# Kernel tuning notes

Measured on AMD Instinct MI355X. Metric: run time of the kernel, lower is better.

## Reference

```python
import jax, jax.numpy as jnp
import numpy as np

ORDER = 64
DT = 1.0 / 2048.0
L, BATCH, SIZE = 2048, 8, 64


def _hippo_legt(N):
    # HiPPO-LegT (LMU) continuous-time transition, as in s4 repo transition()
    Q = np.arange(N, dtype=np.float64)
    R = (2 * Q + 1) ** 0.5
    j, i = np.meshgrid(Q, Q)
    A = R[:, None] * np.where(i < j, (-1.0) ** (i - j), 1.0) * R[None, :]
    B = R[:, None]
    return -A, B


def _bilinear_discretize(A, B, dt):
    # scipy.signal.cont2discrete(..., method='bilinear')
    N = A.shape[0]
    I = np.eye(N)
    M = np.linalg.inv(I - (dt / 2.0) * A)
    Ad = M @ (I + (dt / 2.0) * A)
    Bd = M @ (dt * B)
    return Ad, Bd


def setup_inputs() -> dict:
    key = jax.random.key(0)
    inputs = jax.random.normal(key, (L, BATCH, SIZE), dtype=jnp.float32)
    Ac, Bc = _hippo_legt(ORDER)
    Ad, Bd = _bilinear_discretize(Ac, Bc, DT)
    return {
        "inputs": inputs,
        "A": jnp.asarray(Ad, dtype=jnp.float32),   # (order, order) discrete transition
        "Bm": jnp.asarray(Bd, dtype=jnp.float32),  # (order, 1) discrete input matrix
    }


def reference(inputs, A, Bm):
    # inputs: (L, B, S); A: (N, N); Bm: (N, 1)
    # u = F.linear(inputs.unsqueeze(-1), Bm): u[l,b,s,n] = inputs[l,b,s] * Bm[n,0]
    u = inputs[..., None] * Bm[:, 0]  # (L, B, S, N)

    # parallel_unroll_recursive computes x_t = A x_{t-1} + u_t with x_{-1} = 0
    def step(x, u_t):
        x_new = jnp.einsum('nm,bsm->bsn', A, x) + u_t
        return x_new, x_new

    x0 = jnp.zeros((inputs.shape[1], inputs.shape[2], A.shape[0]), dtype=inputs.dtype)
    _, out = jax.lax.scan(step, x0, u)
    return out  # (L, B, S, N)
```

## Files before the change

### kernel.cpp

```cpp
#include <hip/hip_runtime.h>


typedef _Float16 f16;
typedef __attribute__((ext_vector_type(8))) _Float16 f16x8;
typedef __attribute__((ext_vector_type(4))) float f32x4;

__global__ __launch_bounds__(1024) void kA_pow(
    const float* __restrict__ A, const float* __restrict__ Bm,
    const float* __restrict__ inp,
    float* __restrict__ A64, float* __restrict__ Kv,
    f16* __restrict__ W16, f16* __restrict__ R16)
{
  __shared__ __align__(16) char sA[92160];
  int t = threadIdx.x;

  if (blockIdx.x >= 64) {
    float (*tile)[132] = (float (*)[132])sA;
    int bb = blockIdx.x - 64;
    int j = bb >> 2, qb = (bb & 3) * 128;
    {
      int k = t >> 4, seg = (t & 15) * 8;
      const float* src = inp + j * 32768 + k * 512 + qb + seg;
      *(f32x4*)(&tile[k][seg])     = *(const f32x4*)(src);
      *(f32x4*)(&tile[k][seg + 4]) = *(const f32x4*)(src + 4);
    }
    __syncthreads();
    {
      int q = t & 127, ks8 = (t >> 7) * 8;
      f16 tmp[8];
      #pragma unroll
      for (int kk = 0; kk < 8; ++kk)
        tmp[kk] = (f16)tile[ks8 + kk][q];
      *(f16x8*)(R16 + ((size_t)(j * 512 + qb + q)) * 256 + ks8) =
          *(const f16x8*)tmp;
    }
    return;
  }

  f16 (*Ah)[72]  = (f16 (*)[72])(sA + 0 * 9216);
  f16 (*Al)[72]  = (f16 (*)[72])(sA + 1 * 9216);
  f16 (*B0h)[72] = (f16 (*)[72])(sA + 2 * 9216);
  f16 (*B0l)[72] = (f16 (*)[72])(sA + 3 * 9216);
  f16 (*B1h)[72] = (f16 (*)[72])(sA + 4 * 9216);
  f16 (*B1l)[72] = (f16 (*)[72])(sA + 5 * 9216);
  f16 (*Y8h)[72] = (f16 (*)[72])(sA + 6 * 9216);
  f16 (*Y8l)[72] = (f16 (*)[72])(sA + 7 * 9216);
  f16 (*Ybh)[72] = (f16 (*)[72])(sA + 8 * 9216);
  f16 (*Ybl)[72] = (f16 (*)[72])(sA + 9 * 9216);

  int tau = blockIdx.x;
  int e = tau + 1;
  int a = e >> 3, b = e & 7;
  int wave = t >> 6, lane = t & 63;
  int tn = wave >> 2, tm = wave & 3;
  int kg = lane >> 4, fr = lane & 15;

  auto mm = [&](f16 (*Ph)[72], f16 (*Pl)[72], f16 (*Qh)[72], f16 (*Ql)[72],
                f16 (*Dh)[72], f16 (*Dl)[72]) {
    f32x4 acc = {};
    #pragma unroll
    for (int kk = 0; kk < 2; ++kk) {
      f16x8 ah = *(const f16x8*)&Ph[tn * 16 + fr][kk * 32 + kg * 8];
      f16x8 al = *(const f16x8*)&Pl[tn * 16 + fr][kk * 32 + kg * 8];
      f16x8 bh = *(const f16x8*)&Qh[tm * 16 + fr][kk * 32 + kg * 8];
      f16x8 bl = *(const f16x8*)&Ql[tm * 16 + fr][kk * 32 + kg * 8];
      acc = __builtin_amdgcn_mfma_f32_16x16x32_f16(ah, bh, acc, 0, 0, 0);
      acc = __builtin_amdgcn_mfma_f32_16x16x32_f16(ah, bl, acc, 0, 0, 0);
      acc = __builtin_amdgcn_mfma_f32_16x16x32_f16(al, bh, acc, 0, 0, 0);
    }
    #pragma unroll
    for (int r = 0; r < 4; ++r) {
      float v = acc[r];
      f16 h = (f16)v, l = (f16)(v - (float)h);
      Dh[tn * 16 + kg * 4 + r][tm * 16 + fr] = h;
      Dl[tn * 16 + kg * 4 + r][tm * 16 + fr] = l;
    }
    __syncthreads();
  };
  auto cpy2 = [&](f16 (*Sh)[72], f16 (*Sl)[72], f16 (*Dh)[72], f16 (*Dl)[72]) {
    const unsigned* sh = (const unsigned*)Sh; unsigned* dh = (unsigned*)Dh;
    const unsigned* sl = (const unsigned*)Sl; unsigned* dl = (unsigned*)Dl;
    for (int idx = t; idx < 2304; idx += 1024) { dh[idx] = sh[idx]; dl[idx] = sl[idx]; }
  };

  for (int idx = t; idx < 4096; idx += 1024) {
    float v = A[idx];
    int r = idx >> 6, c2 = idx & 63;
    f16 h = (f16)v, l = (f16)(v - (float)h);
    Ah[r][c2] = h;  Al[r][c2] = l;
    B0h[c2][r] = h; B0l[c2][r] = l;
  }
  __syncthreads();

  f16 (*curH)[72] = B0h; f16 (*curL)[72] = B0l;
  f16 (*othH)[72] = B1h; f16 (*othL)[72] = B1l;
  auto swp = [&]() {
    f16 (*tH)[72] = curH; curH = othH; othH = tH;
    f16 (*tL)[72] = curL; curL = othL; othL = tL;
  };

  if (b == 1) cpy2(curH, curL, Ybh, Ybl);

  int loMax = (a >= 1) ? 8 : b;
  for (int i = 2; i <= loMax; ++i) {
    mm(curH, curL, Ah, Al, othH, othL);
    swp();
    if (i == b) cpy2(curH, curL, Ybh, Ybl);
    if (i == 8) cpy2(curH, curL, Y8h, Y8l);
  }

  f16 (*Rh)[72]; f16 (*Rl)[72]; bool tr;
  if (a == 0) {
    Rh = curH; Rl = curL; tr = true;
  } else {
    for (int idx = t; idx < 4096; idx += 1024) {
      int i = idx >> 6, j = idx & 63;
      othH[i][j] = curH[j][i];
      othL[i][j] = curL[j][i];
    }
    swp();
    __syncthreads();
    for (int a2 = 2; a2 <= a; ++a2) {
      mm(curH, curL, Y8h, Y8l, othH, othL);
      swp();
    }
    if (b >= 1) {
      mm(curH, curL, Ybh, Ybl, othH, othL);
      swp();
    }
    Rh = curH; Rl = curL; tr = false;
  }

  for (int idx = t; idx < 4096; idx += 1024) {
    int wn = idx >> 6, m = idx & 63;
    f16 h = tr ? Rh[m][wn] : Rh[wn][m];
    f16 l = tr ? Rl[m][wn] : Rl[wn][m];
    f16* wrow = W16 + ((size_t)(tau * 64 + wn)) * 256;
    wrow[64 + m] = h; wrow[128 + m] = l; wrow[192 + m] = h;
    if (tau == 63) A64[idx] = (float)h + (float)l;
  }
  if (t < 64) {
    float s = 0.f;
    #pragma unroll 8
    for (int m = 0; m < 64; ++m) {
      float pv = tr ? ((float)Rh[m][t] + (float)Rl[m][t])
                    : ((float)Rh[t][m] + (float)Rl[t][m]);
      s += pv * Bm[m];
    }
    if (tau < 63) Kv[(tau + 1) * 64 + t] = s;
    else          Kv[t] = Bm[t];
  }
}

__global__ __launch_bounds__(256) void kB_prep(
    const float* __restrict__ inp, const float* __restrict__ Kv,
    const float* __restrict__ A64,
    f16* __restrict__ R16, f16* __restrict__ W16)
{
  __shared__ __align__(16) float sm[64 * 66];
  int t = threadIdx.x;
  int b = blockIdx.x;
  if (b < 64) {
    int tau = b;
    for (int idx = t; idx < 4096; idx += 256) sm[idx] = Kv[idx];
    __syncthreads();
    int wn = t & 63, kq = t >> 6;
    f16* wrow = W16 + ((size_t)(tau * 64 + wn)) * 256 + kq * 16;
    #pragma unroll
    for (int ki = 0; ki < 16; ++ki) {
      int k = kq * 16 + ki;
      wrow[ki] = (f16)((k <= tau) ? sm[(tau - k) * 64 + wn] : 0.0f);
    }
  } else {
    int wv = t >> 6, L = t & 63;
    int q = (b - 64) * 4 + wv;
    float* xs = sm + wv * 144;
    float* vs = xs + 72;
    float ar[64], kvr[64];
    #pragma unroll
    for (int m = 0; m < 64; m += 4) {
      f32x4 v4 = *(const f32x4*)(A64 + L * 64 + m);
      ar[m] = v4.x; ar[m + 1] = v4.y; ar[m + 2] = v4.z; ar[m + 3] = v4.w;
    }
    #pragma unroll
    for (int k = 0; k < 64; ++k) kvr[k] = Kv[(63 - k) * 64 + L];
    float x = 0.f;
    float v = inp[(size_t)L * 512 + q];
    for (int j = 0; j < 32; ++j) {
      float vn = (j < 31) ? inp[(size_t)((j + 1) * 64 + L) * 512 + q] : 0.f;
      f16 hh = (f16)x, ll = (f16)(x - (float)hh);
      f16* row = R16 + ((size_t)(j * 512 + q)) * 256;
      row[64 + L] = hh; row[128 + L] = hh; row[192 + L] = ll;
      xs[L] = x;
      vs[L] = v;
      float a0 = 0.f, a1 = 0.f, c0 = 0.f, c1 = 0.f;
      #pragma unroll
      for (int m = 0; m < 64; m += 4) {
        f32x4 xv = *(const f32x4*)(xs + m);
        f32x4 vv = *(const f32x4*)(vs + m);
        a0 += ar[m] * xv.x + ar[m + 1] * xv.y;
        a1 += ar[m + 2] * xv.z + ar[m + 3] * xv.w;
        c0 += kvr[m] * vv.x + kvr[m + 1] * vv.y;
        c1 += kvr[m + 2] * vv.z + kvr[m + 3] * vv.w;
      }
      x = (a0 + a1) + (c0 + c1);
      v = vn;
    }
  }
}

#define STAGEK(ks, dA, dB)                                                      \
  { _Pragma("unroll")                                                           \
    for (int it = 0; it < 4; ++it) {                                            \
      int rr = w32 + it * 8 + r8;                                               \
      __builtin_amdgcn_global_load_lds(                                         \
        (const __attribute__((address_space(1))) void*)                         \
          (R16 + ((size_t)(mtb + rr)) * 256 + (ks) * 64 + swc),                 \
        (__attribute__((address_space(3))) void*)((dA) + (w4 + it) * 512),      \
        16, 0, 0);                                                              \
      __builtin_amdgcn_global_load_lds(                                         \
        (const __attribute__((address_space(1))) void*)                         \
          (W16 + ((size_t)(ntb + rr)) * 256 + (ks) * 64 + swc),                 \
        (__attribute__((address_space(3))) void*)((dB) + (w4 + it) * 512),      \
        16, 0, 0);                                                              \
    } }

#define KSTEP(sA, sB)                                                           \
  { _Pragma("unroll")                                                           \
    for (int kk = 0; kk < 2; ++kk) {                                            \
      f16x8 af[4], bf[4];                                                       \
      _Pragma("unroll")                                                         \
      for (int i = 0; i < 4; ++i) {                                             \
        af[i] = *(const f16x8*)((sA) + (wr * 64 + i * 16 + fr) * 64 + colk[kk]);\
        bf[i] = *(const f16x8*)((sB) + (wc * 64 + i * 16 + fr) * 64 + colk[kk]);\
      }                                                                         \
      _Pragma("unroll")                                                         \
      for (int mi = 0; mi < 4; ++mi)                                            \
        _Pragma("unroll")                                                       \
        for (int ni = 0; ni < 4; ++ni)                                          \
          acc[mi][ni] = __builtin_amdgcn_mfma_f32_16x16x32_f16(                 \
              af[mi], bf[ni], acc[mi][ni], 0, 0, 0);                            \
    } }

#define WAITVM() asm volatile("s_waitcnt vmcnt(0)" ::: "memory")

__global__ __launch_bounds__(256, 4) void kC_gemm(
    const f16* __restrict__ R16, const f16* __restrict__ W16,
    float* __restrict__ out)
{
  __shared__ __align__(16) char smem[34816];
  f16* A0 = (f16*)smem;
  f16* B0 = A0 + 8192;
  float (*stg)[68] = (float (*)[68])smem;

  int wg = blockIdx.x;
  int swz = (wg & 7) * 512 + (wg >> 3);
  int mt = swz >> 5, nt = swz & 31;
  int t = threadIdx.x, w = t >> 6, lane = t & 63;
  int wr = w >> 1, wc = w & 1;
  int kg = lane >> 4, fr = lane & 15;
  int f7 = fr & 7;

  int r8 = lane >> 3, c8 = lane & 7;
  int w32 = w * 32, w4 = w * 4;
  int mtb = mt * 128, ntb = nt * 128;
  int swc = 8 * (c8 ^ r8);

  int colk[2];
  colk[0] = (kg ^ f7) * 8;
  colk[1] = ((4 + kg) ^ f7) * 8;

  f32x4 acc[4][4] = {};

  #pragma unroll
  for (int ks = 0; ks < 4; ++ks) {
    STAGEK(ks, A0, B0);
    WAITVM();
    __syncthreads();
    KSTEP(A0, B0);
    __syncthreads();
  }

  int j = mt >> 2, q0 = (mt & 3) * 128;
  #pragma unroll
  for (int half = 0; half < 2; ++half) {
    if (wc == half) {
      #pragma unroll
      for (int mi = 0; mi < 4; ++mi)
        #pragma unroll
        for (int ni = 0; ni < 4; ++ni)
          #pragma unroll
          for (int r = 0; r < 4; ++r)
            stg[wr * 64 + mi * 16 + kg * 4 + r][ni * 16 + fr] = acc[mi][ni][r];
    }
    __syncthreads();
    int tau_g = nt * 2 + half;
    float* obase = out + (size_t)j * 2097152 + (size_t)tau_g * 32768 + (size_t)q0 * 64;
    #pragma unroll
    for (int it = 0; it < 8; ++it) {
      int fi = it * 1024 + t * 4;
      int rr = fi >> 6, cc = fi & 63;
      __builtin_nontemporal_store(*(const f32x4*)(&stg[rr][cc]),
                                  (f32x4*)(obase + fi));
    }
    __syncthreads();
  }
}

extern "C" void kernel_launch(void* const* d_in, const int* in_sizes, int n_in,
                              void* d_out, int out_size, void* d_ws, size_t ws_size,
                              hipStream_t stream)
{
  (void)in_sizes; (void)n_in; (void)out_size; (void)ws_size;
  const float* inp = (const float*)d_in[0];
  const float* A   = (const float*)d_in[1];
  const float* Bm  = (const float*)d_in[2];
  float* out = (float*)d_out;

  float* ws = (float*)d_ws;
  float* A64 = ws;
  float* Kv  = ws + 4096;
  f16*  W16  = (f16*)(ws + 8192);
  f16*  R16  = (f16*)((char*)d_ws + 2129920);

  hipLaunchKernelGGL(kA_pow,  dim3(192),  dim3(1024), 0, stream, A, Bm, inp, A64, Kv, W16, R16);
  hipLaunchKernelGGL(kB_prep, dim3(192),  dim3(256),  0, stream, inp, Kv, A64, R16, W16);
  hipLaunchKernelGGL(kC_gemm, dim3(4096), dim3(256),  0, stream, R16, W16, out);
}
```

Baseline: 102.8 us.

## Double-buffer GEMM K-loop with 32-wide stages to overlap loads and MFMA

Splits the K dimension of the fp16 MFMA GEMM into eight 32-wide stages and alternates two LDS buffers, so the global-to-LDS load for the next stage is issued before computing on the current one. Partial vmcnt waits and raw s_barrier with sched_barrier replace the full vmcnt(0)+__syncthreads per stage, and a new XOR swizzle matches the 32-column layout. The goal is to hide load latency behind MFMA work. In exchange there are more barriers and smaller k-steps per stage, and the hand-counted vmcnt values must stay correct.

```diff
diff --git a/kernel.cpp b/kernel.cpp
--- a/kernel.cpp
+++ b/kernel.cpp
@@ -209,48 +209,48 @@
   }
 }
 
-#define STAGEK(ks, dA, dB)                                                      \
+#define STAGE32(ks, dbuf)                                                       \
   { _Pragma("unroll")                                                           \
-    for (int it = 0; it < 4; ++it) {                                            \
-      int rr = w32 + it * 8 + r8;                                               \
+    for (int it = 0; it < 2; ++it) {                                            \
       __builtin_amdgcn_global_load_lds(                                         \
         (const __attribute__((address_space(1))) void*)                         \
-          (R16 + ((size_t)(mtb + rr)) * 256 + (ks) * 64 + swc),                 \
-        (__attribute__((address_space(3))) void*)((dA) + (w4 + it) * 512),      \
+          (R16 + ((size_t)(mtb + w32 + it * 16 + l4)) * 256 + (ks) * 32 + swc32),\
+        (__attribute__((address_space(3))) void*)((dbuf) + w * 1024 + it * 512),\
         16, 0, 0);                                                              \
       __builtin_amdgcn_global_load_lds(                                         \
         (const __attribute__((address_space(1))) void*)                         \
-          (W16 + ((size_t)(ntb + rr)) * 256 + (ks) * 64 + swc),                 \
-        (__attribute__((address_space(3))) void*)((dB) + (w4 + it) * 512),      \
+          (W16 + ((size_t)(ntb + w32 + it * 16 + l4)) * 256 + (ks) * 32 + swc32),\
+        (__attribute__((address_space(3))) void*)((dbuf) + 4096 + w * 1024 + it * 512),\
         16, 0, 0);                                                              \
     } }
 
-#define KSTEP(sA, sB)                                                           \
-  { _Pragma("unroll")                                                           \
-    for (int kk = 0; kk < 2; ++kk) {                                            \
-      f16x8 af[4], bf[4];                                                       \
+#define KSTEP32(sbuf)                                                           \
+  { f16x8 af[4], bf[4];                                                         \
+    _Pragma("unroll")                                                           \
+    for (int i = 0; i < 4; ++i) {                                               \
+      af[i] = *(const f16x8*)((sbuf) + (wr * 64 + i * 16 + fr) * 32 + scol);    \
+      bf[i] = *(const f16x8*)((sbuf) + 4096 + (wc * 64 + i * 16 + fr) * 32 + scol);\
+    }                                                                           \
+    _Pragma("unroll")                                                           \
+    for (int mi = 0; mi < 4; ++mi)                                              \
       _Pragma("unroll")                                                         \
-      for (int i = 0; i < 4; ++i) {                                             \
-        af[i] = *(const f16x8*)((sA) + (wr * 64 + i * 16 + fr) * 64 + colk[kk]);\
-        bf[i] = *(const f16x8*)((sB) + (wc * 64 + i * 16 + fr) * 64 + colk[kk]);\
-      }                                                                         \
-      _Pragma("unroll")                                                         \
-      for (int mi = 0; mi < 4; ++mi)                                            \
-        _Pragma("unroll")                                                       \
-        for (int ni = 0; ni < 4; ++ni)                                          \
-          acc[mi][ni] = __builtin_amdgcn_mfma_f32_16x16x32_f16(                 \
-              af[mi], bf[ni], acc[mi][ni], 0, 0, 0);                            \
-    } }
-
-#define WAITVM() asm volatile("s_waitcnt vmcnt(0)" ::: "memory")
+      for (int ni = 0; ni < 4; ++ni)                                            \
+        acc[mi][ni] = __builtin_amdgcn_mfma_f32_16x16x32_f16(                   \
+            af[mi], bf[ni], acc[mi][ni], 0, 0, 0);                              \
+  }
+
+#define WAITN(n) asm volatile("s_waitcnt vmcnt(" #n ")" ::: "memory")
+#define BAR()                                                                   \
+  { __builtin_amdgcn_sched_barrier(0); __builtin_amdgcn_s_barrier();            \
+    __builtin_amdgcn_sched_barrier(0); }
 
 __global__ __launch_bounds__(256, 4) void kC_gemm(
     const f16* __restrict__ R16, const f16* __restrict__ W16,
     float* __restrict__ out)
 {
   __shared__ __align__(16) char smem[34816];
-  f16* A0 = (f16*)smem;
-  f16* B0 = A0 + 8192;
+  f16* b0v = (f16*)smem;
+  f16* b1v = b0v + 8192;
   float (*stg)[68] = (float (*)[68])smem;
 
   int wg = blockIdx.x;
@@ -259,27 +259,24 @@
   int t = threadIdx.x, w = t >> 6, lane = t & 63;
   int wr = w >> 1, wc = w & 1;
   int kg = lane >> 4, fr = lane & 15;
-  int f7 = fr & 7;
-
-  int r8 = lane >> 3, c8 = lane & 7;
-  int w32 = w * 32, w4 = w * 4;
+
+  int l4 = lane >> 2;
+  int swc32 = 8 * ((lane & 3) ^ ((lane >> 3) & 3));
+  int w32 = w * 32;
   int mtb = mt * 128, ntb = nt * 128;
-  int swc = 8 * (c8 ^ r8);
-
-  int colk[2];
-  colk[0] = (kg ^ f7) * 8;
-  colk[1] = ((4 + kg) ^ f7) * 8;
+  int scol = 8 * (kg ^ ((fr >> 1) & 3));
 
   f32x4 acc[4][4] = {};
 
-  #pragma unroll
-  for (int ks = 0; ks < 4; ++ks) {
-    STAGEK(ks, A0, B0);
-    WAITVM();
-    __syncthreads();
-    KSTEP(A0, B0);
-    __syncthreads();
-  }
+  STAGE32(0, b0v);
+  STAGE32(1, b1v); WAITN(4); BAR(); KSTEP32(b0v); BAR();
+  STAGE32(2, b0v); WAITN(4); BAR(); KSTEP32(b1v); BAR();
+  STAGE32(3, b1v); WAITN(4); BAR(); KSTEP32(b0v); BAR();
+  STAGE32(4, b0v); WAITN(4); BAR(); KSTEP32(b1v); BAR();
+  STAGE32(5, b1v); WAITN(4); BAR(); KSTEP32(b0v); BAR();
+  STAGE32(6, b0v); WAITN(4); BAR(); KSTEP32(b1v); BAR();
+  STAGE32(7, b1v); WAITN(4); BAR(); KSTEP32(b0v); BAR();
+  WAITN(0); BAR(); KSTEP32(b1v); BAR();
 
   int j = mt >> 2, q0 = (mt & 3) * 128;
   #pragma unroll
@@ -293,7 +290,8 @@
           for (int r = 0; r < 4; ++r)
             stg[wr * 64 + mi * 16 + kg * 4 + r][ni * 16 + fr] = acc[mi][ni][r];
     }
-    __syncthreads();
+    asm volatile("s_waitcnt lgkmcnt(0)" ::: "memory");
+    BAR();
     int tau_g = nt * 2 + half;
     float* obase = out + (size_t)j * 2097152 + (size_t)tau_g * 32768 + (size_t)q0 * 64;
     #pragma unroll
@@ -303,7 +301,7 @@
       __builtin_nontemporal_store(*(const f32x4*)(&stg[rr][cc]),
                                   (f32x4*)(obase + fi));
     }
-    __syncthreads();
+    BAR();
   }
 }
 
```

After: 100.8 us. 1.02x faster.
